# Optimization experiments

Hardware: AMD Instinct MI355X
Metric: run time of the kernel (lower is better)

The kernel has to match this reference:

```python
import jax, jax.numpy as jnp
import numpy as np

D_X, D_K, D_V = 1024, 128, 128
B, N = 8, 2048


def setup_inputs() -> dict:
    key = jax.random.key(0)
    ks = jax.random.split(key, 7)
    s = lambda fan_in: 1.0 / np.sqrt(fan_in)
    return {
        "x": jax.random.normal(ks[0], (B, N, D_X), dtype=jnp.float32),
        "w_q": jax.random.uniform(ks[1], (D_K, D_X), jnp.float32, -s(D_X), s(D_X)),
        "b_q": jax.random.uniform(ks[2], (D_K,), jnp.float32, -s(D_X), s(D_X)),
        "w_k": jax.random.uniform(ks[3], (D_K, D_X), jnp.float32, -s(D_X), s(D_X)),
        "b_k": jax.random.uniform(ks[4], (D_K,), jnp.float32, -s(D_X), s(D_X)),
        "w_v": jax.random.uniform(ks[5], (D_V, D_X), jnp.float32, -s(D_X), s(D_X)),
        "b_v": jax.random.uniform(ks[6], (D_V,), jnp.float32, -s(D_X), s(D_X)),
    }


def reference(x, w_q, b_q, w_k, b_k, w_v, b_v):
    # Q is computed in the original module but unused; omit (no effect on output).
    K = jnp.einsum('bnx,kx->bnk', x, w_k) + b_k  # [B,N,d_k]
    V = jnp.einsum('bnx,vx->bnv', x, w_v) + b_v  # [B,N,d_v]
    # logits = K @ V^T / sqrt(d_k)  -> [B,N,N]  (note: K vs V, not Q vs K)
    scale = 1.0 / np.sqrt(D_K).astype(np.float32)
    logits = jnp.einsum('bnk,bmk->bnm', K, V) * scale
    attn = jax.nn.softmax(logits, axis=-1)
    return jnp.einsum('bnm,bmv->bnv', attn, V)
```

## Files before the change

kernel.cpp:

```cpp
#include <hip/hip_runtime.h>
#include <hip/hip_bf16.h>


typedef short s16x8 __attribute__((ext_vector_type(8)));
typedef float f32x4 __attribute__((ext_vector_type(4)));
typedef unsigned short u16;

#define AS1 __attribute__((address_space(1)))
#define AS3 __attribute__((address_space(3)))

__device__ __forceinline__ void gld_lds16(const void* g, void* l) {
  __builtin_amdgcn_global_load_lds((const AS1 unsigned int*)g, (AS3 unsigned int*)l, 16, 0, 0);
}

__device__ __forceinline__ float bf2f(u16 u) {
  unsigned int v = ((unsigned int)u) << 16;
  return __builtin_bit_cast(float, v);
}
__device__ __forceinline__ u16 f2bf(float f) {
  unsigned int u = __builtin_bit_cast(unsigned int, f);
  u += 0x7fffu + ((u >> 16) & 1u);
  return (u16)(u >> 16);
}
__device__ __forceinline__ unsigned pack_bf2(float a, float b) {
  unsigned ua = __builtin_bit_cast(unsigned, a) + 0x8000u;
  unsigned ub = __builtin_bit_cast(unsigned, b) + 0x8000u;
  return __builtin_amdgcn_perm(ub, ua, 0x07060302u);
}

__global__ __launch_bounds__(256, 4) void wconv_kernel(
    const float* __restrict__ wk, const float* __restrict__ wv,
    u16* __restrict__ wbf)
{
  const int e = (blockIdx.x * 256 + threadIdx.x) * 8;
  const float* src = (e < 131072) ? (wk + e) : (wv + (e - 131072));
  float4 a = *(const float4*)src;
  float4 b = *(const float4*)(src + 4);
  union { unsigned u[4]; s16x8 v; } pk;
  pk.u[0] = pack_bf2(a.x, a.y); pk.u[1] = pack_bf2(a.z, a.w);
  pk.u[2] = pack_bf2(b.x, b.y); pk.u[3] = pack_bf2(b.z, b.w);
  *(s16x8*)(wbf + e) = pk.v;
}

__global__ __launch_bounds__(512, 2) void kv_gemm_kernel(
    const float* __restrict__ x, const u16* __restrict__ wbf,
    const float* __restrict__ bk, const float* __restrict__ bv,
    u16* __restrict__ Kout, u16* __restrict__ Vout, u16* __restrict__ VTout)
{
  __shared__ u16 sA[2][8 * 512];
  __shared__ u16 sB[4][32 * 512];

  const int tid  = threadIdx.x;
  const int wave = tid >> 6;
  const int lane = tid & 63;
  const int l16  = lane & 15;
  const int lq   = lane >> 4;
  const int row0 = blockIdx.x * 64;
  const int wr   = wave >> 2;
  const int wc   = wave & 3;

  f32x4 acc[2][4];
  for (int i = 0; i < 2; ++i)
    for (int j = 0; j < 4; ++j) acc[i][j] = (f32x4){0.f, 0.f, 0.f, 0.f};

  const int kc = tid & 7, arow = tid >> 3;
  const float* aSrc = x + (size_t)(row0 + arow) * 1024 + kc * 8;
  const int aSlot = (((arow >> 4) * 2 + (kc >> 2)) * 512) + ((kc & 3) * 16 + (arow & 15)) * 8;

  const u16* bSrc[4];
  for (int i = 0; i < 4; ++i) {
    const int sl = wave + i * 8;
    bSrc[i] = wbf + (size_t)((sl >> 1) * 16 + l16) * 1024 + (sl & 1) * 32 + lq * 8;
  }

  for (int i = 0; i < 4; ++i)
    gld_lds16(bSrc[i], &sB[0][(wave + i * 8) * 512]);
  float4 p0a = *(const float4*)(aSrc);
  float4 p0b = *(const float4*)(aSrc + 4);
  for (int i = 0; i < 4; ++i)
    gld_lds16(bSrc[i] + 64, &sB[1][(wave + i * 8) * 512]);
  float4 p1a = *(const float4*)(aSrc + 64);
  float4 p1b = *(const float4*)(aSrc + 68);

#pragma unroll
  for (int s = 0; s < 16; ++s) {
    const int buf2 = s & 1, buf4 = s & 3;
    {
      union { unsigned u[4]; s16x8 v; } pk;
      pk.u[0] = pack_bf2(p0a.x, p0a.y); pk.u[1] = pack_bf2(p0a.z, p0a.w);
      pk.u[2] = pack_bf2(p0b.x, p0b.y); pk.u[3] = pack_bf2(p0b.z, p0b.w);
      *(s16x8*)(&sA[buf2][aSlot]) = pk.v;
    }
    asm volatile("s_waitcnt lgkmcnt(0)" ::: "memory");
    __builtin_amdgcn_s_barrier();
    if (s == 15) asm volatile("s_waitcnt vmcnt(0)" ::: "memory");
    else         asm volatile("s_waitcnt vmcnt(6)" ::: "memory");
    __builtin_amdgcn_sched_barrier(0);

    if (s + 2 < 16) {
      for (int i = 0; i < 4; ++i)
        gld_lds16(bSrc[i] + (s + 2) * 64, &sB[(s + 2) & 3][(wave + i * 8) * 512]);
    }
    p0a = p1a; p0b = p1b;
    if (s + 2 < 16) {
      p1a = *(const float4*)(aSrc + (s + 2) * 64);
      p1b = *(const float4*)(aSrc + (s + 2) * 64 + 4);
    }

    s16x8 af[2][2], bfr[4][2];
    for (int rb = 0; rb < 2; ++rb)
      for (int ks = 0; ks < 2; ++ks)
        af[rb][ks] = *(const s16x8*)(&sA[buf2][(((wr * 2 + rb) * 2 + ks) * 64 + lane) * 8]);
    for (int cb = 0; cb < 4; ++cb)
      for (int ks = 0; ks < 2; ++ks)
        bfr[cb][ks] = *(const s16x8*)(&sB[buf4][(((wc * 4 + cb) * 2 + ks) * 64 + lane) * 8]);
    for (int rb = 0; rb < 2; ++rb)
      for (int cb = 0; cb < 4; ++cb)
        for (int ks = 0; ks < 2; ++ks)
          acc[rb][cb] = __builtin_amdgcn_mfma_f32_16x16x32_bf16(af[rb][ks], bfr[cb][ks], acc[rb][cb], 0, 0, 0);
  }

  const int  colBase = wc * 64;
  const bool isV = (wc >= 2);
  const float vscale = isV ? 1.0f : 0.08838834764831845f;
  u16* outN = isV ? Vout : Kout;
  float fbias[4];
  for (int cb = 0; cb < 4; ++cb) {
    const int col = colBase + cb * 16 + l16;
    fbias[cb] = isV ? bv[col - 128] : bk[col];
  }
  for (int rb = 0; rb < 2; ++rb) {
    const int grow0 = row0 + wr * 32 + rb * 16 + lq * 4;
    for (int cb = 0; cb < 4; ++cb) {
      const int gcol = colBase + cb * 16 + l16;
      const int ocol = isV ? (gcol - 128) : gcol;
      union { u16 u[4]; unsigned long long ull; } pk;
      for (int r = 0; r < 4; ++r) {
        u16 h = f2bf((acc[rb][cb][r] + fbias[cb]) * vscale);
        outN[(size_t)(grow0 + r) * 128 + ocol] = h;
        pk.u[r] = h;
      }
      if (isV) {
        const int bidx = grow0 >> 11;
        const int n    = grow0 & 2047;
        *(unsigned long long*)(VTout + (size_t)bidx * 128 * 2048 + (size_t)ocol * 2048 + n) = pk.ull;
      }
    }
  }
}

__global__ __launch_bounds__(256, 2) void flash_kernel(
    const u16* __restrict__ Kmat, const u16* __restrict__ Vmat,
    const u16* __restrict__ VT, float* __restrict__ out,
    float* __restrict__ Opart, float* __restrict__ lbuf)
{
  __shared__ u16 sV[2][16 * 512];
  __shared__ u16 sVT[2][16 * 512];
  __shared__ u16 sP[64 * 66];

  const int tid  = threadIdx.x;
  const int wave = tid >> 6;
  const int lane = tid & 63;
  const int l16  = lane & 15;
  const int lq   = lane >> 4;
  const int b    = blockIdx.y;
  const int q0   = blockIdx.x * 64;
  const int z    = blockIdx.z;
  const int ntiles = (2048 / gridDim.z) / 64;
  const int mstart = z * (2048 / gridDim.z);

  s16x8 kf[4];
  {
    const u16* Kb = Kmat + ((size_t)b * 2048 + q0 + wave * 16 + l16) * 128 + lq * 8;
    for (int ks = 0; ks < 4; ++ks) kf[ks] = *(const s16x8*)(Kb + ks * 32);
  }

  const u16* vSrc[4];  const u16* vtSrc[4];
  {
    const u16* Vb  = Vmat + (size_t)b * 2048 * 128;
    const u16* VTb = VT   + (size_t)b * 128 * 2048;
    for (int i = 0; i < 4; ++i) {
      const int sl = wave + i * 4;
      vSrc[i]  = Vb  + (size_t)((sl >> 2) * 16 + l16) * 128 + (sl & 3) * 32 + lq * 8;
      vtSrc[i] = VTb + (size_t)((sl >> 1) * 16 + l16) * 2048 + (sl & 1) * 32 + lq * 8;
    }
  }

  f32x4 oacc[8];
  for (int v = 0; v < 8; ++v) oacc[v] = (f32x4){0.f, 0.f, 0.f, 0.f};
  float lrow[4] = {0.f, 0.f, 0.f, 0.f};

  for (int i = 0; i < 4; ++i) {
    gld_lds16(vSrc[i] + (size_t)mstart * 128, &sV[0][(wave + i * 4) * 512]);
    gld_lds16(vtSrc[i] + mstart,              &sVT[0][(wave + i * 4) * 512]);
  }

  for (int mt = 0; mt < ntiles; ++mt) {
    const int buf = mt & 1;
    asm volatile("s_barrier" ::: "memory");
    if (mt + 1 < ntiles) {
      const int m1 = mstart + (mt + 1) * 64;
      for (int i = 0; i < 4; ++i) {
        gld_lds16(vSrc[i] + (size_t)m1 * 128, &sV[buf ^ 1][(wave + i * 4) * 512]);
        gld_lds16(vtSrc[i] + m1,              &sVT[buf ^ 1][(wave + i * 4) * 512]);
      }
      asm volatile("s_waitcnt vmcnt(8)" ::: "memory");
    } else {
      asm volatile("s_waitcnt vmcnt(0)" ::: "memory");
    }
    __builtin_amdgcn_sched_barrier(0);

    f32x4 sacc[4];
    for (int t = 0; t < 4; ++t) sacc[t] = (f32x4){0.f, 0.f, 0.f, 0.f};
    for (int ks = 0; ks < 4; ++ks)
      for (int t = 0; t < 4; ++t)
        sacc[t] = __builtin_amdgcn_mfma_f32_16x16x32_bf16(
            kf[ks], *(const s16x8*)(&sV[buf][(t * 4 + ks) * 512 + lane * 8]), sacc[t], 0, 0, 0);

    for (int r = 0; r < 4; ++r) {
      const int prow = (wave * 16 + lq * 4 + r) * 66;
      float rs = 0.f;
      for (int t = 0; t < 4; ++t) {
        float p = __expf(sacc[t][r]);
        u16 h = f2bf(p);
        sP[prow + t * 16 + l16] = h;
        rs += bf2f(h);
      }
      lrow[r] += rs;
    }

    for (int ksm = 0; ksm < 2; ++ksm) {
      s16x8 a = *(const s16x8*)(&sP[(wave * 16 + l16) * 66 + ksm * 32 + lq * 8]);
      for (int v = 0; v < 8; ++v)
        oacc[v] = __builtin_amdgcn_mfma_f32_16x16x32_bf16(
            a, *(const s16x8*)(&sVT[buf][(v * 2 + ksm) * 512 + lane * 8]), oacc[v], 0, 0, 0);
    }
  }

  for (int r = 0; r < 4; ++r) {
    lrow[r] += __shfl_xor(lrow[r], 1);
    lrow[r] += __shfl_xor(lrow[r], 2);
    lrow[r] += __shfl_xor(lrow[r], 4);
    lrow[r] += __shfl_xor(lrow[r], 8);
  }

  const size_t rowg = (size_t)b * 2048 + q0 + wave * 16;
  if (gridDim.z == 1) {
    for (int r = 0; r < 4; ++r) {
      const float inv = 1.f / lrow[r];
      for (int v = 0; v < 8; ++v)
        out[(rowg + lq * 4 + r) * 128 + v * 16 + l16] = oacc[v][r] * inv;
    }
  } else {
    float* Op = Opart + (size_t)z * 2097152;
    float* lp = lbuf + (size_t)z * 32768;
    for (int r = 0; r < 4; ++r)
      for (int v = 0; v < 8; ++v)
        Op[(rowg + lq * 4 + r) * 128 + v * 16 + l16] = oacc[v][r];
    if (l16 == 0)
      for (int r = 0; r < 4; ++r)
        lp[rowg + lq * 4 + r] = lrow[r];
  }
}

__global__ __launch_bounds__(256, 4) void combine_kernel(
    const float* __restrict__ Opart, const float* __restrict__ lbuf,
    float* __restrict__ out)
{
  const int idx = blockIdx.x * 256 + threadIdx.x;
  const int row = idx >> 5;
  const float4 o0 = ((const float4*)Opart)[idx];
  const float4 o1 = ((const float4*)(Opart + 2097152))[idx];
  const float inv = 1.f / (lbuf[row] + lbuf[32768 + row]);
  float4 o;
  o.x = (o0.x + o1.x) * inv;
  o.y = (o0.y + o1.y) * inv;
  o.z = (o0.z + o1.z) * inv;
  o.w = (o0.w + o1.w) * inv;
  ((float4*)out)[idx] = o;
}

extern "C" void kernel_launch(void* const* d_in, const int* in_sizes, int n_in,
                              void* d_out, int out_size, void* d_ws, size_t ws_size,
                              hipStream_t stream) {
  const float* x  = (const float*)d_in[0];
  const float* wk = (const float*)d_in[3];
  const float* bk = (const float*)d_in[4];
  const float* wv = (const float*)d_in[5];
  const float* bv = (const float*)d_in[6];

  u16* ws   = (u16*)d_ws;
  u16* wbf  = ws;
  u16* Kmat = ws + 262144;
  u16* Vmat = Kmat + (size_t)16384 * 128;
  u16* VTm  = Vmat + (size_t)16384 * 128;
  float* Opart = (float*)(VTm + (size_t)16384 * 128);
  float* lbuf  = Opart + 2 * 2097152;
  const bool split = ws_size >= (size_t)30200000;

  wconv_kernel<<<128, 256, 0, stream>>>(wk, wv, wbf);
  kv_gemm_kernel<<<256, 512, 0, stream>>>(x, wbf, bk, bv, Kmat, Vmat, VTm);
  if (split) {
    flash_kernel<<<dim3(32, 8, 2), 256, 0, stream>>>(Kmat, Vmat, VTm,
                                                     (float*)d_out, Opart, lbuf);
    combine_kernel<<<2048, 256, 0, stream>>>(Opart, lbuf, (float*)d_out);
  } else {
    flash_kernel<<<dim3(32, 8, 1), 256, 0, stream>>>(Kmat, Vmat, VTm,
                                                     (float*)d_out, Opart, lbuf);
  }
}
```

Baseline: 167.9 us.

## Keep softmax probabilities in registers via transposed QK MFMA and lane shuffles

Swaps the MFMA operands in the score computation so each lane holds a transposed score tile. The exponentiated probabilities are then packed to bf16 pairs and redistributed with cross-lane shuffles into the A-operand layout for the PV MFMA, replacing the LDS round trip through the sP buffer. Row sums are reduced across different lanes to match the new layout. This removes LDS writes and reads and frees shared memory, at the cost of 16 shuffles and selects per tile.

New measurement: 164.5 us. -2.0%, faster.

```diff
diff --git a/kernel.cpp b/kernel.cpp
--- a/kernel.cpp
+++ b/kernel.cpp
@@ -156,7 +156,6 @@
 {
   __shared__ u16 sV[2][16 * 512];
   __shared__ u16 sVT[2][16 * 512];
-  __shared__ u16 sP[64 * 66];
 
   const int tid  = threadIdx.x;
   const int wave = tid >> 6;
@@ -169,6 +168,11 @@
   const int ntiles = (2048 / gridDim.z) / 64;
   const int mstart = z * (2048 / gridDim.z);
 
+  const int bq   = lq & 1;
+  const bool ahi = (lq & 2) != 0;
+  const int src0 = l16 + (2 * bq + 0) * 16;
+  const int src1 = l16 + (2 * bq + 1) * 16;
+
   s16x8 kf[4];
   {
     const u16* Kb = Kmat + ((size_t)b * 2048 + q0 + wave * 16 + l16) * 128 + lq * 8;
@@ -188,7 +192,7 @@
 
   f32x4 oacc[8];
   for (int v = 0; v < 8; ++v) oacc[v] = (f32x4){0.f, 0.f, 0.f, 0.f};
-  float lrow[4] = {0.f, 0.f, 0.f, 0.f};
+  float lrow = 0.f;
 
   for (int i = 0; i < 4; ++i) {
     gld_lds16(vSrc[i] + (size_t)mstart * 128, &sV[0][(wave + i * 4) * 512]);
@@ -215,39 +219,59 @@
     for (int ks = 0; ks < 4; ++ks)
       for (int t = 0; t < 4; ++t)
         sacc[t] = __builtin_amdgcn_mfma_f32_16x16x32_bf16(
-            kf[ks], *(const s16x8*)(&sV[buf][(t * 4 + ks) * 512 + lane * 8]), sacc[t], 0, 0, 0);
-
-    for (int r = 0; r < 4; ++r) {
-      const int prow = (wave * 16 + lq * 4 + r) * 66;
-      float rs = 0.f;
-      for (int t = 0; t < 4; ++t) {
-        float p = __expf(sacc[t][r]);
-        u16 h = f2bf(p);
-        sP[prow + t * 16 + l16] = h;
-        rs += bf2f(h);
-      }
-      lrow[r] += rs;
-    }
-
+            *(const s16x8*)(&sV[buf][(t * 4 + ks) * 512 + lane * 8]), kf[ks], sacc[t], 0, 0, 0);
+
+    unsigned D[4][2];
+    float rs = 0.f;
+    for (int t = 0; t < 4; ++t)
+      for (int p = 0; p < 2; ++p) {
+        float e0 = __expf(sacc[t][2 * p]);
+        float e1 = __expf(sacc[t][2 * p + 1]);
+        unsigned d = pack_bf2(e0, e1);
+        D[t][p] = d;
+        rs += bf2f((u16)(d & 0xffffu)) + bf2f((u16)(d >> 16));
+      }
+    lrow += rs;
+
+    s16x8 pa[2];
     for (int ksm = 0; ksm < 2; ++ksm) {
-      s16x8 a = *(const s16x8*)(&sP[(wave * 16 + l16) * 66 + ksm * 32 + lq * 8]);
+      union { unsigned u[4]; s16x8 v; } fr;
+      {
+        unsigned lo = __shfl((int)D[2 * ksm][0], src0);
+        unsigned hi = __shfl((int)D[2 * ksm + 1][0], src0);
+        fr.u[0] = ahi ? hi : lo;
+      }
+      {
+        unsigned lo = __shfl((int)D[2 * ksm][1], src0);
+        unsigned hi = __shfl((int)D[2 * ksm + 1][1], src0);
+        fr.u[1] = ahi ? hi : lo;
+      }
+      {
+        unsigned lo = __shfl((int)D[2 * ksm][0], src1);
+        unsigned hi = __shfl((int)D[2 * ksm + 1][0], src1);
+        fr.u[2] = ahi ? hi : lo;
+      }
+      {
+        unsigned lo = __shfl((int)D[2 * ksm][1], src1);
+        unsigned hi = __shfl((int)D[2 * ksm + 1][1], src1);
+        fr.u[3] = ahi ? hi : lo;
+      }
+      pa[ksm] = fr.v;
+    }
+
+    for (int ksm = 0; ksm < 2; ++ksm)
       for (int v = 0; v < 8; ++v)
         oacc[v] = __builtin_amdgcn_mfma_f32_16x16x32_bf16(
-            a, *(const s16x8*)(&sVT[buf][(v * 2 + ksm) * 512 + lane * 8]), oacc[v], 0, 0, 0);
-    }
-  }
-
-  for (int r = 0; r < 4; ++r) {
-    lrow[r] += __shfl_xor(lrow[r], 1);
-    lrow[r] += __shfl_xor(lrow[r], 2);
-    lrow[r] += __shfl_xor(lrow[r], 4);
-    lrow[r] += __shfl_xor(lrow[r], 8);
-  }
+            pa[ksm], *(const s16x8*)(&sVT[buf][(v * 2 + ksm) * 512 + lane * 8]), oacc[v], 0, 0, 0);
+  }
+
+  lrow += __shfl_xor(lrow, 16);
+  lrow += __shfl_xor(lrow, 32);
 
   const size_t rowg = (size_t)b * 2048 + q0 + wave * 16;
   if (gridDim.z == 1) {
     for (int r = 0; r < 4; ++r) {
-      const float inv = 1.f / lrow[r];
+      const float inv = 1.f / __shfl(lrow, lq * 4 + r);
       for (int v = 0; v < 8; ++v)
         out[(rowg + lq * 4 + r) * 128 + v * 16 + l16] = oacc[v][r] * inv;
     }
@@ -257,9 +281,8 @@
     for (int r = 0; r < 4; ++r)
       for (int v = 0; v < 8; ++v)
         Op[(rowg + lq * 4 + r) * 128 + v * 16 + l16] = oacc[v][r];
-    if (l16 == 0)
-      for (int r = 0; r < 4; ++r)
-        lp[rowg + lq * 4 + r] = lrow[r];
+    if (lq == 0)
+      lp[rowg + l16] = lrow;
   }
 }
 
```
